# Performance work log

Measured on AMD Instinct MI355X. Metric: run time of the kernel, lower is better.

## Reference

```python
import jax, jax.numpy as jnp
import numpy as np
import itertools

EPSILON = 1e-6
OUT_SIZE = 4096
IN_SIZE = 4096
RANK = 2  # in_rank + len(out_shape)
REGION = np.array([16.0, 16.0], dtype=np.float32)
PRIMES = np.array([2, 3], dtype=np.int64)  # first RANK primes from the buffer
# floor/ceil combinations, same order as itertools.product([True, False], repeat=RANK)
FLOOR_MASK = np.array([[int(b) for b in bools] for bools in itertools.product([True, False], repeat=RANK)], dtype=bool)  # (2**RANK, RANK)


def generate_integer_tuples(means, rr_u, g_u, rng_sizes, region):
    # means: (b, k, RANK); rr_u/g_u: uniform(0,1) samples (b, k, radd/gadd, RANK)
    b, k, rank = means.shape
    m = jax.lax.stop_gradient(means)  # torch uses means.data
    mexp = m[:, :, None, :]
    # all floor/ceil corner combinations of the continuous index tuple
    neigh = jnp.where(FLOOR_MASK[None, None, :, :], jnp.floor(mexp), jnp.ceil(mexp)).astype(jnp.int64)
    # uniform samples over the whole index space
    g_ints = jnp.floor(g_u * (1.0 - EPSILON) * rng_sizes).astype(jnp.int64)
    # uniform samples from a small window around round(means)
    mr = jnp.round(mexp)
    lower = mr - region * 0.5
    upper = mr + region * 0.5
    lower = jnp.where(lower < 0.0, 0.0, lower)
    lower = jnp.where(upper > rng_sizes, rng_sizes - region, lower)
    rr_ints = (rr_u * (1.0 - EPSILON) * region + lower).astype(jnp.int64)
    ints = jnp.concatenate([neigh, g_ints, rr_ints], axis=2)  # (b, k, 2**RANK+gadd+radd, RANK)
    return ints.reshape(b, -1, rank)


def duplicates(tuples):
    # tuples: (b, n, r) int64 -> bool mask (b, n) marking all-but-first occurrences
    b, n, r = tuples.shape
    unique = jnp.prod((tuples + 1) ** PRIMES[:r], axis=2)  # prime-power hash
    sort_idx = jnp.argsort(unique, axis=1)
    sorted_v = jnp.take_along_axis(unique, sort_idx, axis=1)
    unsort_idx = jnp.argsort(sort_idx, axis=1)
    mask = jnp.concatenate(
        [jnp.zeros((b, 1), dtype=bool), sorted_v[:, 1:] == sorted_v[:, :-1]], axis=1)
    return jnp.take_along_axis(mask, unsort_idx, axis=1)


def densities(points, means, sigmas):
    # unnormalized diagonal-MVN pdf: exp(-0.5 * sum_r (p_r - m_r)^2 / (eps + sigma_r))
    # expanded quadratic form via einsum to avoid the (b, n, k, r) intermediate
    inv = 1.0 / (EPSILON + sigmas)                                   # (b, k, r)
    a = jnp.einsum('bnr,bkr->bnk', points * points, inv)
    bt = jnp.einsum('bnr,bkr->bnk', points, means * inv)
    c = jnp.sum(means * means * inv, axis=-1)[:, None, :]
    return jnp.exp(-0.5 * (a - 2.0 * bt + c))                        # (b, n, k)


def setup_inputs() -> dict:
    key = jax.random.key(0)
    ks = jax.random.split(key, 7)
    b, k, gadd, radd = 4, 256, 64, 64
    rng = jnp.array([OUT_SIZE, IN_SIZE], dtype=jnp.float32)
    x = jax.random.normal(ks[0], (b, IN_SIZE), dtype=jnp.float32)
    means = jax.random.uniform(ks[1], (b, k, RANK), dtype=jnp.float32) * (rng - 1.0)
    sigmas = (jax.random.uniform(ks[2], (b, k, RANK), dtype=jnp.float32) * 2.0 + 0.5) * (rng / 64.0)
    values = jax.random.normal(ks[3], (b, k), dtype=jnp.float32)
    bias = jax.random.normal(ks[4], (OUT_SIZE,), dtype=jnp.float32)
    rr_u = jax.random.uniform(ks[5], (b, k, radd, RANK), dtype=jnp.float32)
    g_u = jax.random.uniform(ks[6], (b, k, gadd, RANK), dtype=jnp.float32)
    return {"x": x, "means": means, "sigmas": sigmas, "values": values,
            "bias": bias, "rr_u": rr_u, "g_u": g_u}


def reference(x, means, sigmas, values, bias, rr_u, g_u):
    b, in_size = x.shape
    rng_sizes = jnp.array([OUT_SIZE, in_size], dtype=jnp.float32)
    region = jnp.asarray(REGION)
    indices = jax.lax.stop_gradient(
        generate_integer_tuples(means, rr_u, g_u, rng_sizes, region))  # (b, n, 2)
    dups = duplicates(indices)                                        # (b, n) bool
    props = densities(indices.astype(jnp.float32), means, sigmas)     # (b, n, k)
    props = jnp.where(dups[:, :, None], 0.0, props)                   # zero duplicates
    props = props / props.sum(axis=1, keepdims=True)
    weights = jnp.einsum('bnk,bk->bn', props, values)                 # per-index weight
    out_idx = indices[:, :, 0]  # output coordinate (len(out_shape)=1)
    in_idx = indices[:, :, 1]   # input coordinate (in_rank=1)
    gathered = jnp.take_along_axis(x, in_idx, axis=1)                 # (b, n)
    barange = jnp.arange(b)[:, None]
    y = jnp.zeros((b, OUT_SIZE), dtype=x.dtype).at[barange, out_idx].add(weights * gathered)
    return y + bias[None, :]
```

## Files before the change

kernel.cpp:

```cpp
#include <hip/hip_runtime.h>
#include <cstdint>

#define BATCH 4
#define KCOMP 256
#define GADD 64
#define RADD 64
#define PPK 132
#define NPB (KCOMP * PPK)
#define NTOT (BATCH * NPB)
#define OUTS 4096
#define INS 4096
#define TBITS 16
#define TSIZE (1 << TBITS)
#define TILES 132

#define NEG_HALF_LOG2E (-0.72134752044448170f)

#define KEYS_BYTES  ((size_t)BATCH * TSIZE * 8)
#define DENOM_BYTES ((size_t)BATCH * KCOMP * 4)
#define VALS_BYTES  ((size_t)BATCH * TSIZE * 4)
#define PTS_BYTES   ((size_t)NTOT * 4)

#define ZERO_U4 131328
#define FF_U4   65536
#define Y_F4    4096
#define INIT_TOT (ZERO_U4 + FF_U4 + Y_F4)

__device__ __forceinline__ unsigned long long point_hash(long long t0, long long t1) {
    unsigned long long a = (unsigned long long)((t0 + 1) * (t0 + 1));
    unsigned long long b = (unsigned long long)((t1 + 1) * (t1 + 1) * (t1 + 1));
    return a * b;
}

__device__ __forceinline__ unsigned int slot_of(unsigned long long h) {
    return (unsigned int)((h * 0x9E3779B97F4A7C15ull) >> (64 - TBITS));
}

__global__ void k_init(const float* __restrict__ bias, float* __restrict__ y,
                       uint4* __restrict__ zero_base, uint4* __restrict__ ff_base) {
    int i = blockIdx.x * blockDim.x + threadIdx.x;
    if (i < ZERO_U4) {
        zero_base[i] = make_uint4(0u, 0u, 0u, 0u);
    } else if (i < ZERO_U4 + FF_U4) {
        ff_base[i - ZERO_U4] = make_uint4(~0u, ~0u, ~0u, ~0u);
    } else if (i < INIT_TOT) {
        int j = i - (ZERO_U4 + FF_U4);
        float4 bv = ((const float4*)bias)[j & 1023];
        ((float4*)y)[j] = bv;
    }
}

__global__ void k_gen(const float* __restrict__ means,
                      const float* __restrict__ rr_u,
                      const float* __restrict__ g_u,
                      uint32_t* __restrict__ pts,
                      unsigned long long* __restrict__ keys,
                      unsigned int* __restrict__ vals) {
    int n = blockIdx.x * blockDim.x + threadIdx.x;
    if (n >= NTOT) return;
    int b = n / NPB;
    int loc = n - b * NPB;
    int k = loc / PPK;
    int j = loc - k * PPK;

    const float* mp = means + (size_t)(b * KCOMP + k) * 2;
    double m0 = (double)mp[0], m1 = (double)mp[1];
    long long t0, t1;
    if (j < 4) {
        t0 = (long long)((j < 2) ? floor(m0) : ceil(m0));
        t1 = (long long)(((j & 1) == 0) ? floor(m1) : ceil(m1));
    } else if (j < 4 + GADD) {
        int gi = j - 4;
        const float* gp = g_u + ((size_t)((b * KCOMP + k) * GADD) + gi) * 2;
        t0 = (long long)floor((double)gp[0] * (1.0 - 1e-6) * 4096.0);
        t1 = (long long)floor((double)gp[1] * (1.0 - 1e-6) * 4096.0);
    } else {
        int ri = j - 4 - GADD;
        const float* rp = rr_u + ((size_t)((b * KCOMP + k) * RADD) + ri) * 2;
        double mr0 = rint(m0), mr1 = rint(m1);
        double lo0 = mr0 - 8.0;
        if (lo0 < 0.0) lo0 = 0.0;
        if (mr0 + 8.0 > 4096.0) lo0 = 4080.0;
        double lo1 = mr1 - 8.0;
        if (lo1 < 0.0) lo1 = 0.0;
        if (mr1 + 8.0 > 4096.0) lo1 = 4080.0;
        t0 = (long long)((double)rp[0] * (1.0 - 1e-6) * 16.0 + lo0);
        t1 = (long long)((double)rp[1] * (1.0 - 1e-6) * 16.0 + lo1);
    }

    pts[n] = (uint32_t)t0 | ((uint32_t)t1 << 12);

    unsigned long long h = point_hash(t0, t1);
    unsigned long long* kb = keys + (size_t)b * TSIZE;
    unsigned int* vb = vals + (size_t)b * TSIZE;
    unsigned int s = slot_of(h);
    for (;;) {
        unsigned long long prev = atomicCAS(&kb[s], 0ull, h);
        if (prev == 0ull || prev == h) {
            atomicMin(&vb[s], (unsigned int)loc);
            break;
        }
        s = (s + 1) & (TSIZE - 1);
    }
}

__global__ void k_denomA(const float* __restrict__ means,
                         const float* __restrict__ sigmas,
                         uint32_t* __restrict__ pts,
                         const unsigned long long* __restrict__ keys,
                         const unsigned int* __restrict__ vals,
                         float* __restrict__ denom) {
    __shared__ float2 spt[256];
    int bid = blockIdx.x;
    int b = bid / TILES;
    int tile = bid - b * TILES;
    int t = threadIdx.x;
    int loc = tile * 256 + t;

    {
        uint32_t p = pts[(size_t)b * NPB + loc];
        long long t0 = (long long)(p & 0xFFFu);
        long long t1 = (long long)((p >> 12) & 0xFFFu);
        unsigned long long h = point_hash(t0, t1);
        const unsigned long long* kb = keys + (size_t)b * TSIZE;
        const unsigned int* vb = vals + (size_t)b * TSIZE;
        unsigned int s = slot_of(h);
        while (kb[s] != h) s = (s + 1) & (TSIZE - 1);
        if (vb[s] != (unsigned int)loc) {
            pts[(size_t)b * NPB + loc] = p | 0x80000000u;
            spt[t] = make_float2(1.0e9f, 0.0f);
        } else {
            spt[t] = make_float2((float)t0, (float)t1);
        }
    }
    __syncthreads();

    int bk = b * KCOMP + t;
    float m0 = means[bk * 2], m1 = means[bk * 2 + 1];
    float i0 = NEG_HALF_LOG2E / (1e-6f + sigmas[bk * 2]);
    float i1 = NEG_HALF_LOG2E / (1e-6f + sigmas[bk * 2 + 1]);

    float a0 = 0.0f, a1 = 0.0f, a2 = 0.0f, a3 = 0.0f;
#pragma unroll 4
    for (int j = 0; j < 256; j += 4) {
        float2 q0 = spt[j], q1 = spt[j + 1], q2 = spt[j + 2], q3 = spt[j + 3];
        float dx, dy;
        dx = q0.x - m0; dy = q0.y - m1; a0 += exp2f(dx * dx * i0 + dy * dy * i1);
        dx = q1.x - m0; dy = q1.y - m1; a1 += exp2f(dx * dx * i0 + dy * dy * i1);
        dx = q2.x - m0; dy = q2.y - m1; a2 += exp2f(dx * dx * i0 + dy * dy * i1);
        dx = q3.x - m0; dy = q3.y - m1; a3 += exp2f(dx * dx * i0 + dy * dy * i1);
    }
    atomicAdd(&denom[bk], (a0 + a1) + (a2 + a3));
}

__global__ void k_scatterB(const float* __restrict__ means,
                           const float* __restrict__ sigmas,
                           const float* __restrict__ values,
                           const float* __restrict__ denom,
                           const float* __restrict__ x,
                           const uint32_t* __restrict__ pts,
                           float* __restrict__ y) {
    __shared__ float4 prm[KCOMP];
    __shared__ float cf[KCOMP];
    int bid = blockIdx.x;
    int b = bid / TILES;
    int tile = bid - b * TILES;
    int t = threadIdx.x;

    {
        int bk = b * KCOMP + t;
        float i0 = NEG_HALF_LOG2E / (1e-6f + sigmas[bk * 2]);
        float i1 = NEG_HALF_LOG2E / (1e-6f + sigmas[bk * 2 + 1]);
        prm[t] = make_float4(means[bk * 2], means[bk * 2 + 1], i0, i1);
        cf[t] = values[bk] / denom[bk];
    }
    __syncthreads();

    int loc = tile * 256 + t;
    uint32_t p = pts[(size_t)b * NPB + loc];
    if (p & 0x80000000u) return;

    float p0 = (float)(p & 0xFFFu);
    float p1 = (float)((p >> 12) & 0xFFFu);
    float w0 = 0.0f, w1 = 0.0f, w2 = 0.0f, w3 = 0.0f;
#pragma unroll 4
    for (int q = 0; q < KCOMP; q += 4) {
        float4 r0 = prm[q], r1 = prm[q + 1], r2 = prm[q + 2], r3 = prm[q + 3];
        float dx, dy;
        dx = p0 - r0.x; dy = p1 - r0.y;
        w0 = fmaf(exp2f(dx * dx * r0.z + dy * dy * r0.w), cf[q], w0);
        dx = p0 - r1.x; dy = p1 - r1.y;
        w1 = fmaf(exp2f(dx * dx * r1.z + dy * dy * r1.w), cf[q + 1], w1);
        dx = p0 - r2.x; dy = p1 - r2.y;
        w2 = fmaf(exp2f(dx * dx * r2.z + dy * dy * r2.w), cf[q + 2], w2);
        dx = p0 - r3.x; dy = p1 - r3.y;
        w3 = fmaf(exp2f(dx * dx * r3.z + dy * dy * r3.w), cf[q + 3], w3);
    }
    float w = (w0 + w1) + (w2 + w3);
    int out_idx = (int)(p & 0xFFFu);
    int in_idx = (int)((p >> 12) & 0xFFFu);
    atomicAdd(&y[(size_t)b * OUTS + out_idx], w * x[(size_t)b * INS + in_idx]);
}

extern "C" void kernel_launch(void* const* d_in, const int* in_sizes, int n_in,
                              void* d_out, int out_size, void* d_ws, size_t ws_size,
                              hipStream_t stream) {
    const float* x      = (const float*)d_in[0];
    const float* means  = (const float*)d_in[1];
    const float* sigmas = (const float*)d_in[2];
    const float* values = (const float*)d_in[3];
    const float* bias   = (const float*)d_in[4];
    const float* rr_u   = (const float*)d_in[5];
    const float* g_u    = (const float*)d_in[6];
    float* y = (float*)d_out;

    uint8_t* w = (uint8_t*)d_ws;
    unsigned long long* keys = (unsigned long long*)w;
    float* denom = (float*)(w + KEYS_BYTES);
    unsigned int* vals = (unsigned int*)(w + KEYS_BYTES + DENOM_BYTES);
    uint32_t* pts = (uint32_t*)(w + KEYS_BYTES + DENOM_BYTES + VALS_BYTES);

    hipLaunchKernelGGL(k_init, dim3((INIT_TOT + 255) / 256), dim3(256), 0, stream,
                       bias, y, (uint4*)w, (uint4*)(w + KEYS_BYTES + DENOM_BYTES));
    hipLaunchKernelGGL(k_gen, dim3((NTOT + 255) / 256), dim3(256), 0, stream,
                       means, rr_u, g_u, pts, keys, vals);
    hipLaunchKernelGGL(k_denomA, dim3(BATCH * TILES), dim3(256), 0, stream,
                       means, sigmas, pts, keys, vals, denom);
    hipLaunchKernelGGL(k_scatterB, dim3(BATCH * TILES), dim3(256), 0, stream,
                       means, sigmas, values, denom, x, pts, y);
}
```

Before: 136.2 us.

## Shrink point tiles to 128, split components across half-blocks, and coalesce generation reads

Point generation is reindexed so each thread block reads the neighbour, global and region sample arrays contiguously. Thread i maps to a sample slot, and the output position in the points array is computed from it afterwards. The denominator and scatter kernels now use tiles of 128 points, which doubles the block count. In the scatter kernel, two halves of each block each handle 128 of the 256 Gaussian components and combine partial weights through shared memory before a single atomic add. The exp2f with folded log2e is replaced by __expf, and accumulators are unrolled to 8 for more ILP. The trade-off is extra shared-memory reduction and sync, plus more atomic adds to denom.

```diff
diff --git a/kernel.cpp b/kernel.cpp
--- a/kernel.cpp
+++ b/kernel.cpp
@@ -12,9 +12,8 @@
 #define INS 4096
 #define TBITS 16
 #define TSIZE (1 << TBITS)
-#define TILES 132
-
-#define NEG_HALF_LOG2E (-0.72134752044448170f)
+#define TILE 128
+#define TILES (NPB / TILE)
 
 #define KEYS_BYTES  ((size_t)BATCH * TSIZE * 8)
 #define DENOM_BYTES ((size_t)BATCH * KCOMP * 4)
@@ -56,27 +55,28 @@
                       uint32_t* __restrict__ pts,
                       unsigned long long* __restrict__ keys,
                       unsigned int* __restrict__ vals) {
-    int n = blockIdx.x * blockDim.x + threadIdx.x;
-    if (n >= NTOT) return;
-    int b = n / NPB;
-    int loc = n - b * NPB;
-    int k = loc / PPK;
-    int j = loc - k * PPK;
-
-    const float* mp = means + (size_t)(b * KCOMP + k) * 2;
-    double m0 = (double)mp[0], m1 = (double)mp[1];
+    int i = blockIdx.x * blockDim.x + threadIdx.x;
+    int bk, j;
     long long t0, t1;
-    if (j < 4) {
+    if (i < 4096) {
+        bk = i >> 2;
+        j = i & 3;
+        double m0 = (double)means[bk * 2], m1 = (double)means[bk * 2 + 1];
         t0 = (long long)((j < 2) ? floor(m0) : ceil(m0));
         t1 = (long long)(((j & 1) == 0) ? floor(m1) : ceil(m1));
-    } else if (j < 4 + GADD) {
-        int gi = j - 4;
-        const float* gp = g_u + ((size_t)((b * KCOMP + k) * GADD) + gi) * 2;
+    } else if (i < 4096 + 65536) {
+        int i2 = i - 4096;
+        bk = i2 >> 6;
+        j = 4 + (i2 & 63);
+        const float* gp = g_u + (size_t)i2 * 2;
         t0 = (long long)floor((double)gp[0] * (1.0 - 1e-6) * 4096.0);
         t1 = (long long)floor((double)gp[1] * (1.0 - 1e-6) * 4096.0);
     } else {
-        int ri = j - 4 - GADD;
-        const float* rp = rr_u + ((size_t)((b * KCOMP + k) * RADD) + ri) * 2;
+        int i3 = i - (4096 + 65536);
+        bk = i3 >> 6;
+        j = 68 + (i3 & 63);
+        const float* rp = rr_u + (size_t)i3 * 2;
+        double m0 = (double)means[bk * 2], m1 = (double)means[bk * 2 + 1];
         double mr0 = rint(m0), mr1 = rint(m1);
         double lo0 = mr0 - 8.0;
         if (lo0 < 0.0) lo0 = 0.0;
@@ -87,8 +87,10 @@
         t0 = (long long)((double)rp[0] * (1.0 - 1e-6) * 16.0 + lo0);
         t1 = (long long)((double)rp[1] * (1.0 - 1e-6) * 16.0 + lo1);
     }
-
-    pts[n] = (uint32_t)t0 | ((uint32_t)t1 << 12);
+    int b = bk >> 8;
+    int loc = (bk & 255) * PPK + j;
+
+    pts[(size_t)b * NPB + loc] = (uint32_t)t0 | ((uint32_t)t1 << 12);
 
     unsigned long long h = point_hash(t0, t1);
     unsigned long long* kb = keys + (size_t)b * TSIZE;
@@ -110,14 +112,14 @@
                          const unsigned long long* __restrict__ keys,
                          const unsigned int* __restrict__ vals,
                          float* __restrict__ denom) {
-    __shared__ float2 spt[256];
+    __shared__ float2 spt[TILE];
     int bid = blockIdx.x;
     int b = bid / TILES;
     int tile = bid - b * TILES;
     int t = threadIdx.x;
-    int loc = tile * 256 + t;
-
-    {
+
+    if (t < TILE) {
+        int loc = tile * TILE + t;
         uint32_t p = pts[(size_t)b * NPB + loc];
         long long t0 = (long long)(p & 0xFFFu);
         long long t1 = (long long)((p >> 12) & 0xFFFu);
@@ -137,20 +139,25 @@
 
     int bk = b * KCOMP + t;
     float m0 = means[bk * 2], m1 = means[bk * 2 + 1];
-    float i0 = NEG_HALF_LOG2E / (1e-6f + sigmas[bk * 2]);
-    float i1 = NEG_HALF_LOG2E / (1e-6f + sigmas[bk * 2 + 1]);
-
-    float a0 = 0.0f, a1 = 0.0f, a2 = 0.0f, a3 = 0.0f;
+    float i0 = -0.5f / (1e-6f + sigmas[bk * 2]);
+    float i1 = -0.5f / (1e-6f + sigmas[bk * 2 + 1]);
+
+    float a0 = 0.f, a1 = 0.f, a2 = 0.f, a3 = 0.f, a4 = 0.f, a5 = 0.f, a6 = 0.f, a7 = 0.f;
 #pragma unroll 4
-    for (int j = 0; j < 256; j += 4) {
-        float2 q0 = spt[j], q1 = spt[j + 1], q2 = spt[j + 2], q3 = spt[j + 3];
+    for (int j = 0; j < TILE; j += 8) {
+        float2 q0 = spt[j],     q1 = spt[j + 1], q2 = spt[j + 2], q3 = spt[j + 3];
+        float2 q4 = spt[j + 4], q5 = spt[j + 5], q6 = spt[j + 6], q7 = spt[j + 7];
         float dx, dy;
-        dx = q0.x - m0; dy = q0.y - m1; a0 += exp2f(dx * dx * i0 + dy * dy * i1);
-        dx = q1.x - m0; dy = q1.y - m1; a1 += exp2f(dx * dx * i0 + dy * dy * i1);
-        dx = q2.x - m0; dy = q2.y - m1; a2 += exp2f(dx * dx * i0 + dy * dy * i1);
-        dx = q3.x - m0; dy = q3.y - m1; a3 += exp2f(dx * dx * i0 + dy * dy * i1);
-    }
-    atomicAdd(&denom[bk], (a0 + a1) + (a2 + a3));
+        dx = q0.x - m0; dy = q0.y - m1; a0 += __expf(dx * dx * i0 + dy * dy * i1);
+        dx = q1.x - m0; dy = q1.y - m1; a1 += __expf(dx * dx * i0 + dy * dy * i1);
+        dx = q2.x - m0; dy = q2.y - m1; a2 += __expf(dx * dx * i0 + dy * dy * i1);
+        dx = q3.x - m0; dy = q3.y - m1; a3 += __expf(dx * dx * i0 + dy * dy * i1);
+        dx = q4.x - m0; dy = q4.y - m1; a4 += __expf(dx * dx * i0 + dy * dy * i1);
+        dx = q5.x - m0; dy = q5.y - m1; a5 += __expf(dx * dx * i0 + dy * dy * i1);
+        dx = q6.x - m0; dy = q6.y - m1; a6 += __expf(dx * dx * i0 + dy * dy * i1);
+        dx = q7.x - m0; dy = q7.y - m1; a7 += __expf(dx * dx * i0 + dy * dy * i1);
+    }
+    atomicAdd(&denom[bk], ((a0 + a1) + (a2 + a3)) + ((a4 + a5) + (a6 + a7)));
 }
 
 __global__ void k_scatterB(const float* __restrict__ means,
@@ -162,6 +169,7 @@
                            float* __restrict__ y) {
     __shared__ float4 prm[KCOMP];
     __shared__ float cf[KCOMP];
+    __shared__ float wpart[TILE];
     int bid = blockIdx.x;
     int b = bid / TILES;
     int tile = bid - b * TILES;
@@ -169,37 +177,56 @@
 
     {
         int bk = b * KCOMP + t;
-        float i0 = NEG_HALF_LOG2E / (1e-6f + sigmas[bk * 2]);
-        float i1 = NEG_HALF_LOG2E / (1e-6f + sigmas[bk * 2 + 1]);
+        float i0 = -0.5f / (1e-6f + sigmas[bk * 2]);
+        float i1 = -0.5f / (1e-6f + sigmas[bk * 2 + 1]);
         prm[t] = make_float4(means[bk * 2], means[bk * 2 + 1], i0, i1);
         cf[t] = values[bk] / denom[bk];
     }
     __syncthreads();
 
-    int loc = tile * 256 + t;
+    int pt_i = t & (TILE - 1);
+    int kbase = (t >> 7) * 128;
+    int loc = tile * TILE + pt_i;
     uint32_t p = pts[(size_t)b * NPB + loc];
-    if (p & 0x80000000u) return;
-
-    float p0 = (float)(p & 0xFFFu);
-    float p1 = (float)((p >> 12) & 0xFFFu);
-    float w0 = 0.0f, w1 = 0.0f, w2 = 0.0f, w3 = 0.0f;
+    bool live = !(p & 0x80000000u);
+
+    float w = 0.0f;
+    if (live) {
+        float p0 = (float)(p & 0xFFFu);
+        float p1 = (float)((p >> 12) & 0xFFFu);
+        float w0 = 0.f, w1 = 0.f, w2 = 0.f, w3 = 0.f, w4 = 0.f, w5 = 0.f, w6 = 0.f, w7 = 0.f;
 #pragma unroll 4
-    for (int q = 0; q < KCOMP; q += 4) {
-        float4 r0 = prm[q], r1 = prm[q + 1], r2 = prm[q + 2], r3 = prm[q + 3];
-        float dx, dy;
-        dx = p0 - r0.x; dy = p1 - r0.y;
-        w0 = fmaf(exp2f(dx * dx * r0.z + dy * dy * r0.w), cf[q], w0);
-        dx = p0 - r1.x; dy = p1 - r1.y;
-        w1 = fmaf(exp2f(dx * dx * r1.z + dy * dy * r1.w), cf[q + 1], w1);
-        dx = p0 - r2.x; dy = p1 - r2.y;
-        w2 = fmaf(exp2f(dx * dx * r2.z + dy * dy * r2.w), cf[q + 2], w2);
-        dx = p0 - r3.x; dy = p1 - r3.y;
-        w3 = fmaf(exp2f(dx * dx * r3.z + dy * dy * r3.w), cf[q + 3], w3);
-    }
-    float w = (w0 + w1) + (w2 + w3);
-    int out_idx = (int)(p & 0xFFFu);
-    int in_idx = (int)((p >> 12) & 0xFFFu);
-    atomicAdd(&y[(size_t)b * OUTS + out_idx], w * x[(size_t)b * INS + in_idx]);
+        for (int q = kbase; q < kbase + 128; q += 8) {
+            float4 r0 = prm[q],     r1 = prm[q + 1], r2 = prm[q + 2], r3 = prm[q + 3];
+            float4 r4 = prm[q + 4], r5 = prm[q + 5], r6 = prm[q + 6], r7 = prm[q + 7];
+            float dx, dy;
+            dx = p0 - r0.x; dy = p1 - r0.y;
+            w0 = fmaf(__expf(dx * dx * r0.z + dy * dy * r0.w), cf[q],     w0);
+            dx = p0 - r1.x; dy = p1 - r1.y;
+            w1 = fmaf(__expf(dx * dx * r1.z + dy * dy * r1.w), cf[q + 1], w1);
+            dx = p0 - r2.x; dy = p1 - r2.y;
+            w2 = fmaf(__expf(dx * dx * r2.z + dy * dy * r2.w), cf[q + 2], w2);
+            dx = p0 - r3.x; dy = p1 - r3.y;
+            w3 = fmaf(__expf(dx * dx * r3.z + dy * dy * r3.w), cf[q + 3], w3);
+            dx = p0 - r4.x; dy = p1 - r4.y;
+            w4 = fmaf(__expf(dx * dx * r4.z + dy * dy * r4.w), cf[q + 4], w4);
+            dx = p0 - r5.x; dy = p1 - r5.y;
+            w5 = fmaf(__expf(dx * dx * r5.z + dy * dy * r5.w), cf[q + 5], w5);
+            dx = p0 - r6.x; dy = p1 - r6.y;
+            w6 = fmaf(__expf(dx * dx * r6.z + dy * dy * r6.w), cf[q + 6], w6);
+            dx = p0 - r7.x; dy = p1 - r7.y;
+            w7 = fmaf(__expf(dx * dx * r7.z + dy * dy * r7.w), cf[q + 7], w7);
+        }
+        w = ((w0 + w1) + (w2 + w3)) + ((w4 + w5) + (w6 + w7));
+    }
+    if (t >= TILE) wpart[pt_i] = w;
+    __syncthreads();
+    if (t < TILE && live) {
+        w += wpart[pt_i];
+        int out_idx = (int)(p & 0xFFFu);
+        int in_idx = (int)((p >> 12) & 0xFFFu);
+        atomicAdd(&y[(size_t)b * OUTS + out_idx], w * x[(size_t)b * INS + in_idx]);
+    }
 }
 
 extern "C" void kernel_launch(void* const* d_in, const int* in_sizes, int n_in,
```

Measured after the change: 132.1 us. -3.0%, faster.
